# Performance work log

Measured on AMD Instinct MI355X. Metric: run time of the kernel, lower is better.

Reference implementation:

```python
import jax, jax.numpy as jnp
import numpy as np

HIDDEN = 10

def setup_inputs() -> dict:
    key = jax.random.key(0)
    ks = jax.random.split(key, 12)
    B, T = 4096, 2048
    s_in = 1.0 / np.sqrt(HIDDEN)  # PyTorch RNN/Linear default init scale
    inp = {
        "x": jax.random.normal(ks[0], (B, T, 1), dtype=jnp.float32),
        "hidden_state": jax.random.normal(ks[1], (2, B, HIDDEN), dtype=jnp.float32),
        # layer 0 (input_size=1)
        "W_ih0": jax.random.uniform(ks[2], (HIDDEN, 1), jnp.float32, -s_in, s_in),
        "W_hh0": jax.random.uniform(ks[3], (HIDDEN, HIDDEN), jnp.float32, -s_in, s_in),
        "b_ih0": jax.random.uniform(ks[4], (HIDDEN,), jnp.float32, -s_in, s_in),
        "b_hh0": jax.random.uniform(ks[5], (HIDDEN,), jnp.float32, -s_in, s_in),
        # layer 1 (input_size=HIDDEN)
        "W_ih1": jax.random.uniform(ks[6], (HIDDEN, HIDDEN), jnp.float32, -s_in, s_in),
        "W_hh1": jax.random.uniform(ks[7], (HIDDEN, HIDDEN), jnp.float32, -s_in, s_in),
        "b_ih1": jax.random.uniform(ks[8], (HIDDEN,), jnp.float32, -s_in, s_in),
        "b_hh1": jax.random.uniform(ks[9], (HIDDEN,), jnp.float32, -s_in, s_in),
        # output Linear(10, 1)
        "W_out": jax.random.uniform(ks[10], (1, HIDDEN), jnp.float32, -s_in, s_in),
        "b_out": jax.random.uniform(ks[11], (1,), jnp.float32, -s_in, s_in),
    }
    return inp


def reference(x, hidden_state, W_ih0, W_hh0, b_ih0, b_hh0,
              W_ih1, W_hh1, b_ih1, b_hh1, W_out, b_out):
    # x: [B, T, 1]; hidden_state: [2, B, H]
    h0_init, h1_init = hidden_state[0], hidden_state[1]  # [B, H] each
    xs = jnp.swapaxes(x, 0, 1)  # [T, B, 1] for scan over time

    def step(carry, xt):
        h0, h1 = carry
        h0n = jnp.tanh(xt @ W_ih0.T + b_ih0 + h0 @ W_hh0.T + b_hh0)
        h1n = jnp.tanh(h0n @ W_ih1.T + b_ih1 + h1 @ W_hh1.T + b_hh1)
        return (h0n, h1n), h1n

    (h0_f, h1_f), ys = jax.lax.scan(step, (h0_init, h1_init), xs)  # ys: [T, B, H]
    rnn_output = jnp.swapaxes(ys, 0, 1)  # [B, T, H]
    outs = rnn_output @ W_out.T + b_out  # [B, T, 1] (fused per-timestep Linear)
    hidden_out = jnp.stack([h0_f, h1_f], axis=0)  # [2, B, H]
    return outs, hidden_out
```

## Files before the change

### kernel.cpp

```cpp
#include <hip/hip_runtime.h>

#define HID 10
#define TT  2048
#define BB  4096

typedef float f2 __attribute__((ext_vector_type(2)));

static __device__ __forceinline__ f2 pkmul(f2 a, f2 b) {
    f2 d; asm("v_pk_mul_f32 %0, %1, %2" : "=v"(d) : "v"(a), "v"(b)); return d;
}
static __device__ __forceinline__ f2 pkfma(f2 a, f2 b, f2 c) {
    f2 d; asm("v_pk_fma_f32 %0, %1, %2, %3" : "=v"(d) : "v"(a), "v"(b), "v"(c)); return d;
}

__device__ __forceinline__ float fast_tanh(float x) {
    float e = exp2f(x * 2.885390081777926814f);
    float r = __builtin_amdgcn_rcpf(e + 1.0f);
    return fmaf(-2.0f, r, 1.0f);
}

#define PKDOT(ACC, W, H)                 \
    ACC = pkmul(W[0], H[0]);             \
    ACC = pkfma(W[1], H[1], ACC);        \
    ACC = pkfma(W[2], H[2], ACC);        \
    ACC = pkfma(W[3], H[3], ACC);        \
    ACC = pkfma(W[4], H[4], ACC);

__global__ void __launch_bounds__(128) rnn_kernel(
    const float* __restrict__ x,    const float* __restrict__ hs,
    const float* __restrict__ Wih0, const float* __restrict__ Whh0,
    const float* __restrict__ bih0, const float* __restrict__ bhh0,
    const float* __restrict__ Wih1, const float* __restrict__ Whh1,
    const float* __restrict__ bih1, const float* __restrict__ bhh1,
    const float* __restrict__ Wout, const float* __restrict__ boutp,
    float* __restrict__ out)
{
    const int tid  = threadIdx.x;
    const bool isA = tid < 64;
    const int lane = tid & 15;
    const int grp  = (tid >> 4) & 3;
    const int row  = blockIdx.x * 4 + grp;
    const bool act = (lane < HID);
    const bool ol  = (lane == HID);

    __shared__ float lds[4 * 296];
    const int pg = ((grp << 1) | (grp >> 1)) & 3;
    float* base = &lds[pg * 296];
    float* up   = base + lane;
    float* h0b  = base + 256;
    float* h1b  = base + 280;

    const float* xrow = x   + (size_t)row * TT;
    float*       orow = out + (size_t)row * TT;

    f2 W0[5], W1[5], W2[5], H0[5], H1[5];
    float wih0i = 0.f, b0c = 0.f, ub = 0.f, obias = 0.f;
    float hown = 0.f;
    float4 xa = make_float4(0,0,0,0), xb = make_float4(0,0,0,0);
    float P1 = 0.f, P2 = 0.f;

    if (isA) {
        #pragma unroll
        for (int j = 0; j < 5; ++j) {
            W0[j] = act ? f2{Whh0[lane*HID + 2*j], Whh0[lane*HID + 2*j+1]}
                        : f2{0.f, 0.f};
            W1[j] = act ? f2{Wih1[lane*HID + 2*j], Wih1[lane*HID + 2*j+1]}
                        : f2{0.f, 0.f};
            H0[j] = f2{hs[row*HID + 2*j], hs[row*HID + 2*j+1]};
        }
        wih0i = act ? Wih0[lane] : 0.f;
        b0c   = act ? (bih0[lane] + bhh0[lane]) : 0.f;
        ub    = act ? (bih1[lane] + bhh1[lane]) : (ol ? boutp[0] : 0.f);
        hown  = act ? hs[row*HID + lane] : 0.f;
        xa = *(const float4*)(xrow);
        xb = *(const float4*)(xrow + 4);
    } else {
        #pragma unroll
        for (int j = 0; j < 5; ++j) {
            W2[j] = act ? f2{Whh1[lane*HID + 2*j], Whh1[lane*HID + 2*j+1]}
                  : (ol ? f2{Wout[2*j], Wout[2*j+1]} : f2{0.f, 0.f});
            H1[j] = f2{hs[BB*HID + row*HID + 2*j], hs[BB*HID + row*HID + 2*j+1]};
        }
        obias = ol ? boutp[0] : 0.f;
    }

    for (int m = 0; m <= 256; ++m) {
        if (isA) {
            if (m <= 255) {
                const int mn = (m + 1 <= 255) ? m + 1 : 255;
                const float4 xn0 = *(const float4*)(xrow + 8 * mn);
                const float4 xn1 = *(const float4*)(xrow + 8 * mn + 4);
                const float xs[8] = {xa.x, xa.y, xa.z, xa.w,
                                     xb.x, xb.y, xb.z, xb.w};
                const int sb = (m & 1) * 8;
                #pragma unroll
                for (int k = 0; k < 8; ++k) {
                    __builtin_amdgcn_s_setprio(1);
                    f2 ac; PKDOT(ac, W0, H0);
                    const float s0 = fmaf(xs[k], wih0i, b0c);
                    hown = fast_tanh((s0 + ac.x) + ac.y);
                    h0b[lane] = hown;
                    __builtin_amdgcn_s_setprio(0);
                    __builtin_amdgcn_wave_barrier();
                    const float4 r0 = *(const float4*)(h0b);
                    const float4 r1 = *(const float4*)(h0b + 4);
                    const f2     r2 = *(const f2*)(h0b + 8);
                    f2 uc; PKDOT(uc, W1, H0);
                    up[((sb + k + 15) & 15) * 16] = (ub + uc.x) + uc.y;
                    H0[0] = f2{r0.x, r0.y}; H0[1] = f2{r0.z, r0.w};
                    H0[2] = f2{r1.x, r1.y}; H0[3] = f2{r1.z, r1.w};
                    H0[4] = r2;
                }
                xa = xn0; xb = xn1;
            }
        } else {
            if (m >= 1) {
                const int bb = (m & 1) ? 15 : 7;
                float u[8];
                #pragma unroll
                for (int k = 0; k < 8; ++k)
                    u[k] = up[((bb + k) & 15) * 16];
                float c[8];
                #pragma unroll
                for (int k = 0; k < 8; ++k) {
                    __builtin_amdgcn_s_setprio(1);
                    f2 ac; PKDOT(ac, W2, H1);
                    const float s1 = (u[k] + ac.x) + ac.y;
                    c[k] = s1;
                    const float hn = fast_tanh(s1);
                    h1b[lane] = hn;
                    __builtin_amdgcn_s_setprio(0);
                    __builtin_amdgcn_wave_barrier();
                    const float4 q0 = *(const float4*)(h1b);
                    const float4 q1 = *(const float4*)(h1b + 4);
                    const f2     q2 = *(const f2*)(h1b + 8);
                    if (k > 0 || m > 1) {
                        H1[0] = f2{q0.x, q0.y}; H1[1] = f2{q0.z, q0.w};
                        H1[2] = f2{q1.x, q1.y}; H1[3] = f2{q1.z, q1.w};
                        H1[4] = q2;
                    }
                }
                if (ol) {
                    if (m == 1) {
                        *(float4*)(orow) = make_float4(c[2], c[3], c[4], c[5]);
                    } else {
                        *(float4*)(orow + 8*m - 12) = make_float4(P1, P2, c[0], c[1]);
                        *(float4*)(orow + 8*m - 8)  = make_float4(c[2], c[3], c[4], c[5]);
                    }
                }
                P1 = c[6]; P2 = c[7];
            }
        }
        __syncthreads();
    }

    if (isA) {
        f2 uc; PKDOT(uc, W1, H0);
        up[15 * 16] = (ub + uc.x) + uc.y;
    }
    __syncthreads();
    if (!isA) {
        const float u47 = up[15 * 16];
        f2 ac; PKDOT(ac, W2, H1);
        const float sA = (u47 + ac.x) + ac.y;
        const float h1f = fast_tanh(sA);
        h1b[lane] = h1f;
        __builtin_amdgcn_wave_barrier();
        const float4 q0 = *(const float4*)(h1b);
        const float4 q1 = *(const float4*)(h1b + 4);
        const f2     q2 = *(const f2*)(h1b + 8);
        H1[0] = f2{q0.x, q0.y}; H1[1] = f2{q0.z, q0.w};
        H1[2] = f2{q1.x, q1.y}; H1[3] = f2{q1.z, q1.w};
        H1[4] = q2;
        f2 a2; PKDOT(a2, W2, H1);
        const float o47 = (obias + a2.x) + a2.y;
        if (ol)
            *(float4*)(orow + TT - 4) = make_float4(P1, P2, sA, o47);
        if (act)
            out[(size_t)BB*TT + (size_t)BB*HID + (size_t)row*HID + lane] = h1f;
    } else {
        if (act)
            out[(size_t)BB*TT + (size_t)row*HID + lane] = hown;
    }
}

extern "C" void kernel_launch(void* const* d_in, const int* in_sizes, int n_in,
                              void* d_out, int out_size, void* d_ws, size_t ws_size,
                              hipStream_t stream) {
    const float* x    = (const float*)d_in[0];
    const float* hs   = (const float*)d_in[1];
    const float* Wih0 = (const float*)d_in[2];
    const float* Whh0 = (const float*)d_in[3];
    const float* bih0 = (const float*)d_in[4];
    const float* bhh0 = (const float*)d_in[5];
    const float* Wih1 = (const float*)d_in[6];
    const float* Whh1 = (const float*)d_in[7];
    const float* bih1 = (const float*)d_in[8];
    const float* bhh1 = (const float*)d_in[9];
    const float* Wout = (const float*)d_in[10];
    const float* bout = (const float*)d_in[11];
    float* out = (float*)d_out;

    dim3 grid(BB / 4), block(128);
    hipLaunchKernelGGL(rnn_kernel, grid, block, 0, stream,
        x, hs, Wih0, Whh0, bih0, bhh0, Wih1, Whh1, bih1, bhh1, Wout, bout, out);
}
```

Before: 263.2 us.

## Widen layer pipeline chunk to 32 steps and split recurrent dot-product chains

```diff
diff --git a/kernel.cpp b/kernel.cpp
--- a/kernel.cpp
+++ b/kernel.cpp
@@ -25,6 +25,13 @@
     ACC = pkfma(W[2], H[2], ACC);        \
     ACC = pkfma(W[3], H[3], ACC);        \
     ACC = pkfma(W[4], H[4], ACC);
+
+#define PKDOT2(A0, A1, W, H)             \
+    A0 = pkmul(W[0], H[0]);              \
+    A1 = pkmul(W[1], H[1]);              \
+    A0 = pkfma(W[2], H[2], A0);          \
+    A1 = pkfma(W[3], H[3], A1);          \
+    A0 = pkfma(W[4], H[4], A0);
 
 __global__ void __launch_bounds__(128) rnn_kernel(
     const float* __restrict__ x,    const float* __restrict__ hs,
@@ -43,12 +50,12 @@
     const bool act = (lane < HID);
     const bool ol  = (lane == HID);
 
-    __shared__ float lds[4 * 296];
+    __shared__ float lds[4 * 1064];
     const int pg = ((grp << 1) | (grp >> 1)) & 3;
-    float* base = &lds[pg * 296];
+    float* base = &lds[pg * 1064];
     float* up   = base + lane;
-    float* h0b  = base + 256;
-    float* h1b  = base + 280;
+    float* h0b  = base + 1024;
+    float* h1b  = base + 1040;
 
     const float* xrow = x   + (size_t)row * TT;
     float*       orow = out + (size_t)row * TT;
@@ -56,7 +63,7 @@
     f2 W0[5], W1[5], W2[5], H0[5], H1[5];
     float wih0i = 0.f, b0c = 0.f, ub = 0.f, obias = 0.f;
     float hown = 0.f;
-    float4 xa = make_float4(0,0,0,0), xb = make_float4(0,0,0,0);
+    float4 xq0, xq1, xq2, xq3, xq4, xq5, xq6, xq7;
     float P1 = 0.f, P2 = 0.f;
 
     if (isA) {
@@ -72,8 +79,10 @@
         b0c   = act ? (bih0[lane] + bhh0[lane]) : 0.f;
         ub    = act ? (bih1[lane] + bhh1[lane]) : (ol ? boutp[0] : 0.f);
         hown  = act ? hs[row*HID + lane] : 0.f;
-        xa = *(const float4*)(xrow);
-        xb = *(const float4*)(xrow + 4);
+        xq0 = *(const float4*)(xrow);      xq1 = *(const float4*)(xrow + 4);
+        xq2 = *(const float4*)(xrow + 8);  xq3 = *(const float4*)(xrow + 12);
+        xq4 = *(const float4*)(xrow + 16); xq5 = *(const float4*)(xrow + 20);
+        xq6 = *(const float4*)(xrow + 24); xq7 = *(const float4*)(xrow + 28);
     } else {
         #pragma unroll
         for (int j = 0; j < 5; ++j) {
@@ -84,21 +93,30 @@
         obias = ol ? boutp[0] : 0.f;
     }
 
-    for (int m = 0; m <= 256; ++m) {
+    for (int m = 0; m <= 64; ++m) {
         if (isA) {
-            if (m <= 255) {
-                const int mn = (m + 1 <= 255) ? m + 1 : 255;
-                const float4 xn0 = *(const float4*)(xrow + 8 * mn);
-                const float4 xn1 = *(const float4*)(xrow + 8 * mn + 4);
-                const float xs[8] = {xa.x, xa.y, xa.z, xa.w,
-                                     xb.x, xb.y, xb.z, xb.w};
-                const int sb = (m & 1) * 8;
+            if (m <= 63) {
+                const int mn = (m + 1 <= 63) ? m + 1 : 63;
+                const float4 n0 = *(const float4*)(xrow + 32 * mn);
+                const float4 n1 = *(const float4*)(xrow + 32 * mn + 4);
+                const float4 n2 = *(const float4*)(xrow + 32 * mn + 8);
+                const float4 n3 = *(const float4*)(xrow + 32 * mn + 12);
+                const float4 n4 = *(const float4*)(xrow + 32 * mn + 16);
+                const float4 n5 = *(const float4*)(xrow + 32 * mn + 20);
+                const float4 n6 = *(const float4*)(xrow + 32 * mn + 24);
+                const float4 n7 = *(const float4*)(xrow + 32 * mn + 28);
+                const float xs[32] = {
+                    xq0.x, xq0.y, xq0.z, xq0.w, xq1.x, xq1.y, xq1.z, xq1.w,
+                    xq2.x, xq2.y, xq2.z, xq2.w, xq3.x, xq3.y, xq3.z, xq3.w,
+                    xq4.x, xq4.y, xq4.z, xq4.w, xq5.x, xq5.y, xq5.z, xq5.w,
+                    xq6.x, xq6.y, xq6.z, xq6.w, xq7.x, xq7.y, xq7.z, xq7.w};
+                const int sb = (m & 1) * 32;
                 #pragma unroll
-                for (int k = 0; k < 8; ++k) {
+                for (int k = 0; k < 32; ++k) {
                     __builtin_amdgcn_s_setprio(1);
-                    f2 ac; PKDOT(ac, W0, H0);
+                    f2 a0, a1; PKDOT2(a0, a1, W0, H0);
                     const float s0 = fmaf(xs[k], wih0i, b0c);
-                    hown = fast_tanh((s0 + ac.x) + ac.y);
+                    hown = fast_tanh(((s0 + a0.x) + a0.y) + (a1.x + a1.y));
                     h0b[lane] = hown;
                     __builtin_amdgcn_s_setprio(0);
                     __builtin_amdgcn_wave_barrier();
@@ -106,26 +124,27 @@
                     const float4 r1 = *(const float4*)(h0b + 4);
                     const f2     r2 = *(const f2*)(h0b + 8);
                     f2 uc; PKDOT(uc, W1, H0);
-                    up[((sb + k + 15) & 15) * 16] = (ub + uc.x) + uc.y;
+                    up[((sb + k + 63) & 63) * 16] = (ub + uc.x) + uc.y;
                     H0[0] = f2{r0.x, r0.y}; H0[1] = f2{r0.z, r0.w};
                     H0[2] = f2{r1.x, r1.y}; H0[3] = f2{r1.z, r1.w};
                     H0[4] = r2;
                 }
-                xa = xn0; xb = xn1;
+                xq0 = n0; xq1 = n1; xq2 = n2; xq3 = n3;
+                xq4 = n4; xq5 = n5; xq6 = n6; xq7 = n7;
             }
         } else {
             if (m >= 1) {
-                const int bb = (m & 1) ? 15 : 7;
-                float u[8];
+                const int sbB = ((m - 1) & 1) * 32;
+                float u[32];
                 #pragma unroll
-                for (int k = 0; k < 8; ++k)
-                    u[k] = up[((bb + k) & 15) * 16];
-                float c[8];
+                for (int k = 0; k < 32; ++k)
+                    u[k] = up[((sbB + k + 63) & 63) * 16];
+                float c[32];
                 #pragma unroll
-                for (int k = 0; k < 8; ++k) {
+                for (int k = 0; k < 32; ++k) {
                     __builtin_amdgcn_s_setprio(1);
-                    f2 ac; PKDOT(ac, W2, H1);
-                    const float s1 = (u[k] + ac.x) + ac.y;
+                    f2 a0, a1; PKDOT2(a0, a1, W2, H1);
+                    const float s1 = ((u[k] + a0.x) + a0.y) + (a1.x + a1.y);
                     c[k] = s1;
                     const float hn = fast_tanh(s1);
                     h1b[lane] = hn;
@@ -142,13 +161,20 @@
                 }
                 if (ol) {
                     if (m == 1) {
-                        *(float4*)(orow) = make_float4(c[2], c[3], c[4], c[5]);
+                        #pragma unroll
+                        for (int t = 0; t < 7; ++t)
+                            *(float4*)(orow + 4*t) =
+                                make_float4(c[4*t+2], c[4*t+3], c[4*t+4], c[4*t+5]);
                     } else {
-                        *(float4*)(orow + 8*m - 12) = make_float4(P1, P2, c[0], c[1]);
-                        *(float4*)(orow + 8*m - 8)  = make_float4(c[2], c[3], c[4], c[5]);
+                        const int tb = 32 * m - 36;
+                        *(float4*)(orow + tb) = make_float4(P1, P2, c[0], c[1]);
+                        #pragma unroll
+                        for (int t = 0; t < 7; ++t)
+                            *(float4*)(orow + tb + 4 + 4*t) =
+                                make_float4(c[4*t+2], c[4*t+3], c[4*t+4], c[4*t+5]);
                     }
                 }
-                P1 = c[6]; P2 = c[7];
+                P1 = c[30]; P2 = c[31];
             }
         }
         __syncthreads();
@@ -156,11 +182,11 @@
 
     if (isA) {
         f2 uc; PKDOT(uc, W1, H0);
-        up[15 * 16] = (ub + uc.x) + uc.y;
+        up[63 * 16] = (ub + uc.x) + uc.y;
     }
     __syncthreads();
     if (!isA) {
-        const float u47 = up[15 * 16];
+        const float u47 = up[63 * 16];
         f2 ac; PKDOT(ac, W2, H1);
         const float sA = (u47 + ac.x) + ac.y;
         const float h1f = fast_tanh(sA);
```

Result: no change. 260.1 us (-1.2%).
